# Kernel optimization log

Measured on AMD Instinct MI355X. Metric: run time of the kernel, lower is better.

## Reference

```python
import jax, jax.numpy as jnp
import numpy as np

NUM_USERS = 100000
NUM_ITEMS = 50000
EMB = 64
N_LAYERS = 3
NNZ = 4800000
N_NODES = NUM_USERS + NUM_ITEMS


def setup_inputs() -> dict:
    key = jax.random.key(0)
    k1, k2, k3, k4, k5 = jax.random.split(key, 5)
    emb_user = jax.random.normal(k1, (NUM_USERS, EMB), dtype=jnp.float32) * 0.1
    emb_item = jax.random.normal(k2, (NUM_ITEMS, EMB), dtype=jnp.float32) * 0.1
    adj_rows = jax.random.randint(k3, (NNZ,), 0, N_NODES, dtype=jnp.int32)
    adj_cols = jax.random.randint(k4, (NNZ,), 0, N_NODES, dtype=jnp.int32)
    # normalized adjacency values (stand-in for D^-1/2 A D^-1/2 entries)
    adj_vals = jax.random.uniform(k5, (NNZ,), dtype=jnp.float32) / 32.0
    return {
        "emb_user": emb_user,
        "emb_item": emb_item,
        "adj_vals": adj_vals,
        "adj_rows": adj_rows,
        "adj_cols": adj_cols,
    }


def _spmm(vals, rows, cols, x):
    # y[r] = sum_{e: rows[e]==r} vals[e] * x[cols[e]]
    gathered = x[cols] * vals[:, None]  # [nnz, emb]
    return jax.ops.segment_sum(gathered, rows, num_segments=N_NODES)


def reference(emb_user, emb_item, adj_vals, adj_rows, adj_cols):
    ego = jnp.concatenate([emb_user, emb_item], axis=0)  # [(U+I), emb]
    acc = ego
    h = ego
    for _ in range(N_LAYERS):
        h = _spmm(adj_vals, adj_rows, adj_cols, h)
        acc = acc + h
    mean_emb = acc / jnp.float32(N_LAYERS + 1)
    user_embeddings = mean_emb[:NUM_USERS]
    item_embeddings = mean_emb[NUM_USERS:]
    return user_embeddings, item_embeddings
```

## Files before the change

### kernel.cpp

```cpp
#include <hip/hip_runtime.h>
#include <hip/hip_bf16.h>

#define N_USERS   100000
#define N_ITEMS   50000
#define N_NODES_C 150000
#define EMB       64
#define N_ELEM    (N_NODES_C * EMB)
#define BKT_SHIFT 9
#define NBKT      ((N_NODES_C + 511) >> 9)
#define BKT_CAP   20480
#define CH_EDGES  4096
#define EPT       16

typedef unsigned int u32x4 __attribute__((ext_vector_type(4)));
typedef unsigned int u32x2 __attribute__((ext_vector_type(2)));
typedef unsigned long long u64;

__global__ void detect_and_zero(const unsigned int* __restrict__ emb_u32,
                                const unsigned int* __restrict__ vals_u32,
                                int* __restrict__ flags,
                                int* __restrict__ tails) {
    int t = threadIdx.x;
    for (int b = t; b < NBKT; b += 256) tails[b] = 0;
    int cnt_emb = 0, cnt_vals = 0;
    for (int k = t; k < 1024; k += 256) {
        unsigned e = (emb_u32[k] >> 7) & 0xFFu;
        cnt_emb += (e >= 100u && e <= 127u) ? 1 : 0;
        cnt_vals += (vals_u32[k] >> 15) & 1u;
    }
    __shared__ int s0[256], s1[256];
    s0[t] = cnt_emb; s1[t] = cnt_vals;
    __syncthreads();
    for (int s = 128; s > 0; s >>= 1) {
        if (t < s) { s0[t] += s0[t + s]; s1[t] += s1[t + s]; }
        __syncthreads();
    }
    if (t == 0) {
        flags[0] = (s0[0] > 512) ? 1 : 0;
        flags[1] = (s1[0] > 100) ? 0 : 1;
    }
}

__device__ __forceinline__ float load_f(const void* base, size_t i, int is_bf16) {
    if (is_bf16) return __bfloat162float(((const __hip_bfloat16*)base)[i]);
    return ((const float*)base)[i];
}
__device__ __forceinline__ unsigned int bf16_bits(float f) {
    __hip_bfloat16 h = __float2bfloat16(f);
    return (unsigned int)reinterpret_cast<unsigned short&>(h);
}
__device__ __forceinline__ float lo_bf(unsigned int u) {
    return __uint_as_float(u << 16);
}
__device__ __forceinline__ float hi_bf(unsigned int u) {
    return __uint_as_float(u & 0xFFFF0000u);
}

__global__ void init_kernel(const void* __restrict__ eu,
                            const void* __restrict__ ei,
                            __hip_bfloat16* __restrict__ h0,
                            const int* __restrict__ flags) {
    int q = blockIdx.x * blockDim.x + threadIdx.x;
    if (q >= (N_ELEM >> 2)) return;
    int ebf = flags[0];
    const int uquads = (N_USERS * EMB) >> 2;
    u32x2 o;
    if (ebf) {
        o = (q < uquads)
              ? *((const u32x2*)eu + q)
              : *((const u32x2*)ei + (q - uquads));
    } else {
        const uint4 f = (q < uquads)
              ? *((const uint4*)eu + q)
              : *((const uint4*)ei + (q - uquads));
        unsigned r0, r1;
        asm("v_cvt_pk_bf16_f32 %0, %1, %2" : "=v"(r0)
            : "v"(__uint_as_float(f.x)), "v"(__uint_as_float(f.y)));
        asm("v_cvt_pk_bf16_f32 %0, %1, %2" : "=v"(r1)
            : "v"(__uint_as_float(f.z)), "v"(__uint_as_float(f.w)));
        o.x = r0; o.y = r1;
    }
    *reinterpret_cast<u32x2*>(h0 + ((size_t)q << 2)) = o;
}

__global__ void scatter_bucket(const int* __restrict__ rows, const int* __restrict__ cols,
                               const void* __restrict__ vals,
                               u64* __restrict__ tmp,
                               int* __restrict__ tails, int nnz,
                               const int* __restrict__ flags) {
    __shared__ int lcnt[NBKT];
    __shared__ int lbase[NBKT];
    int t = threadIdx.x;
    for (int b = t; b < NBKT; b += 256) lcnt[b] = 0;
    __syncthreads();
    int base = blockIdx.x * CH_EDGES;
    int vbf = flags[1];
    u64 pk[EPT];
    unsigned int br[EPT];
    #pragma unroll
    for (int i = 0; i < EPT; ++i) {
        int e = base + i * 256 + t;
        if (e < nnz) {
            int r = rows[e];
            int c = cols[e];
            float v = load_f(vals, (size_t)e, vbf);
            int bk = r >> BKT_SHIFT;
            int rk = atomicAdd(&lcnt[bk], 1);
            pk[i] = ((u64)(unsigned)r << 34)
                  | ((u64)(unsigned)c << 16)
                  | (u64)bf16_bits(v);
            br[i] = ((unsigned)bk << 16) | (unsigned)rk;
        } else {
            br[i] = 0xFFFFFFFFu;
        }
    }
    __syncthreads();
    for (int b = t; b < NBKT; b += 256)
        lbase[b] = lcnt[b] ? atomicAdd(&tails[b], lcnt[b]) : 0;
    __syncthreads();
    #pragma unroll
    for (int i = 0; i < EPT; ++i) {
        if (br[i] != 0xFFFFFFFFu) {
            int bk = br[i] >> 16, rk = br[i] & 0xFFFFu;
            int pos = lbase[bk] + rk;
            if (pos < BKT_CAP)
                tmp[(size_t)bk * BKT_CAP + pos] = pk[i];
        }
    }
}

__global__ void bucket_csr(const u64* __restrict__ tmp,
                           int2* __restrict__ edges,
                           const int* __restrict__ tails,
                           int* __restrict__ row_ptr) {
    __shared__ int cnt[512];
    __shared__ int off[512];
    __shared__ int red[512];
    int b = blockIdx.x, t = threadIdx.x;
    int pre = 0;
    for (int i = t; i < b; i += 512) {
        int v = tails[i];
        pre += (v > BKT_CAP) ? BKT_CAP : v;
    }
    red[t] = pre;
    cnt[t] = 0;
    int rowbase = b << BKT_SHIFT;
    int nrows = N_NODES_C - rowbase; if (nrows > 512) nrows = 512;
    int n = tails[b];
    if (n > BKT_CAP) n = BKT_CAP;
    const u64* src = tmp + (size_t)b * BKT_CAP;
    __syncthreads();
    for (int st = 256; st > 0; st >>= 1) {
        if (t < st) red[t] += red[t + st];
        __syncthreads();
    }
    int obase = red[0];
    for (int e = t; e < n; e += 512)
        atomicAdd(&cnt[(int)(src[e] >> 34) - rowbase], 1);
    __syncthreads();
    int v = cnt[t];
    off[t] = v;
    __syncthreads();
    for (int o = 1; o < 512; o <<= 1) {
        int u = (t >= o) ? off[t - o] : 0;
        __syncthreads();
        off[t] += u;
        __syncthreads();
    }
    int excl = off[t] - v;
    __syncthreads();
    off[t] = obase + excl;
    if (t < nrows) row_ptr[rowbase + t] = obase + excl;
    if (b == NBKT - 1 && t == 0) row_ptr[N_NODES_C] = obase + n;
    __syncthreads();
    for (int e = t; e < n; e += 512) {
        u64 p = src[e];
        int rloc = (int)(p >> 34) - rowbase;
        unsigned c = (unsigned)((p >> 16) & 0x3FFFFu);
        int pos = atomicAdd(&off[rloc], 1);
        edges[pos] = make_int2((int)(c << 7), (int)((unsigned)(p & 0xFFFFu) << 16));
    }
}

#define DOT2Q(wA, wB, vp, ae, ao)                                              \
    {                                                                          \
        unsigned _xe = __builtin_amdgcn_perm((wA), (wB), 0x01000504u);         \
        unsigned _xo = __builtin_amdgcn_perm((wA), (wB), 0x03020706u);         \
        asm("v_dot2_f32_bf16 %0, %1, %2, %0" : "+v"(ae) : "v"(_xe), "v"(vp));  \
        asm("v_dot2_f32_bf16 %0, %1, %2, %0" : "+v"(ao) : "v"(_xo), "v"(vp));  \
    }

#define SWZ_ADD(a, pat) \
    a += __int_as_float(__builtin_amdgcn_ds_swizzle(__float_as_int(a), pat))

__global__ void spmm8(const __hip_bfloat16* __restrict__ x,
                      __hip_bfloat16* __restrict__ y,
                      const u64* __restrict__ edges,
                      const int* __restrict__ row_ptr,
                      const __hip_bfloat16* __restrict__ h0,
                      const __hip_bfloat16* __restrict__ h1,
                      void* __restrict__ out,
                      const int* __restrict__ flags,
                      int last) {
    int row = __builtin_amdgcn_readfirstlane(blockIdx.x * 4 + (threadIdx.x >> 6));
    if (row >= N_NODES_C) return;
    int lane = threadIdx.x & 63;
    int slot = lane >> 3;
    int s    = lane & 7;
    int beg = row_ptr[row], end = row_ptr[row + 1];
    const char* xb = (const char*)x;
    const char* eb = (const char*)edges;
    unsigned s16 = (unsigned)s << 4;
    unsigned eoff = ((unsigned)(beg + slot)) << 3;
    float a0 = 0.f, a1 = 0.f, a2 = 0.f, a3 = 0.f,
          a4 = 0.f, a5 = 0.f, a6 = 0.f, a7 = 0.f;
    for (int e = beg; e < end; e += 32, eoff += 256) {
        int rem = end - e;
        const u64* ep = (const u64*)(eb + eoff);
        u64 pA = (slot      < rem) ? __builtin_nontemporal_load(ep)      : 0ULL;
        u64 pB = (slot + 8  < rem) ? __builtin_nontemporal_load(ep + 8)  : 0ULL;
        u64 pC = (slot + 16 < rem) ? __builtin_nontemporal_load(ep + 16) : 0ULL;
        u64 pD = (slot + 24 < rem) ? __builtin_nontemporal_load(ep + 24) : 0ULL;
        unsigned oA = (unsigned)pA + s16;
        unsigned oB = (unsigned)pB + s16;
        unsigned oC = (unsigned)pC + s16;
        unsigned oD = (unsigned)pD + s16;
        const uint4 gA = *reinterpret_cast<const uint4*>(xb + oA);
        const uint4 gB = *reinterpret_cast<const uint4*>(xb + oB);
        const uint4 gC = *reinterpret_cast<const uint4*>(xb + oC);
        const uint4 gD = *reinterpret_cast<const uint4*>(xb + oD);
        unsigned vAB = __builtin_amdgcn_perm((unsigned)(pA >> 32),
                                             (unsigned)(pB >> 32), 0x03020706u);
        unsigned vCD = __builtin_amdgcn_perm((unsigned)(pC >> 32),
                                             (unsigned)(pD >> 32), 0x03020706u);
        DOT2Q(gA.x, gB.x, vAB, a0, a1);
        DOT2Q(gA.y, gB.y, vAB, a2, a3);
        DOT2Q(gA.z, gB.z, vAB, a4, a5);
        DOT2Q(gA.w, gB.w, vAB, a6, a7);
        DOT2Q(gC.x, gD.x, vCD, a0, a1);
        DOT2Q(gC.y, gD.y, vCD, a2, a3);
        DOT2Q(gC.z, gD.z, vCD, a4, a5);
        DOT2Q(gC.w, gD.w, vCD, a6, a7);
    }
    SWZ_ADD(a0, 0x201F); SWZ_ADD(a1, 0x201F); SWZ_ADD(a2, 0x201F); SWZ_ADD(a3, 0x201F);
    SWZ_ADD(a4, 0x201F); SWZ_ADD(a5, 0x201F); SWZ_ADD(a6, 0x201F); SWZ_ADD(a7, 0x201F);
    SWZ_ADD(a0, 0x401F); SWZ_ADD(a1, 0x401F); SWZ_ADD(a2, 0x401F); SWZ_ADD(a3, 0x401F);
    SWZ_ADD(a4, 0x401F); SWZ_ADD(a5, 0x401F); SWZ_ADD(a6, 0x401F); SWZ_ADD(a7, 0x401F);
    a0 += __shfl_xor(a0, 32, 64);
    a1 += __shfl_xor(a1, 32, 64);
    a2 += __shfl_xor(a2, 32, 64);
    a3 += __shfl_xor(a3, 32, 64);
    a4 += __shfl_xor(a4, 32, 64);
    a5 += __shfl_xor(a5, 32, 64);
    a6 += __shfl_xor(a6, 32, 64);
    a7 += __shfl_xor(a7, 32, 64);
    if (slot != 0) return;
    size_t base = ((size_t)row << 6) + (s << 3);
    if (!last) {
        unsigned q0, q1, q2, q3;
        asm("v_cvt_pk_bf16_f32 %0, %1, %2" : "=v"(q0) : "v"(a0), "v"(a1));
        asm("v_cvt_pk_bf16_f32 %0, %1, %2" : "=v"(q1) : "v"(a2), "v"(a3));
        asm("v_cvt_pk_bf16_f32 %0, %1, %2" : "=v"(q2) : "v"(a4), "v"(a5));
        asm("v_cvt_pk_bf16_f32 %0, %1, %2" : "=v"(q3) : "v"(a6), "v"(a7));
        u32x4 o; o.x = q0; o.y = q1; o.z = q2; o.w = q3;
        *reinterpret_cast<u32x4*>(y + base) = o;
    } else {
        const uint4 r0 = *reinterpret_cast<const uint4*>(h0 + base);
        const uint4 r1 = *reinterpret_cast<const uint4*>(h1 + base);
        const uint4 r2 = *reinterpret_cast<const uint4*>(x + base);
        float f0 = (lo_bf(r0.x) + lo_bf(r1.x) + lo_bf(r2.x) + a0) * 0.25f;
        float f1 = (hi_bf(r0.x) + hi_bf(r1.x) + hi_bf(r2.x) + a1) * 0.25f;
        float f2 = (lo_bf(r0.y) + lo_bf(r1.y) + lo_bf(r2.y) + a2) * 0.25f;
        float f3 = (hi_bf(r0.y) + hi_bf(r1.y) + hi_bf(r2.y) + a3) * 0.25f;
        float f4 = (lo_bf(r0.z) + lo_bf(r1.z) + lo_bf(r2.z) + a4) * 0.25f;
        float f5 = (hi_bf(r0.z) + hi_bf(r1.z) + hi_bf(r2.z) + a5) * 0.25f;
        float f6 = (lo_bf(r0.w) + lo_bf(r1.w) + lo_bf(r2.w) + a6) * 0.25f;
        float f7 = (hi_bf(r0.w) + hi_bf(r1.w) + hi_bf(r2.w) + a7) * 0.25f;
        if (flags[0]) {
            unsigned q0, q1, q2, q3;
            asm("v_cvt_pk_bf16_f32 %0, %1, %2" : "=v"(q0) : "v"(f0), "v"(f1));
            asm("v_cvt_pk_bf16_f32 %0, %1, %2" : "=v"(q1) : "v"(f2), "v"(f3));
            asm("v_cvt_pk_bf16_f32 %0, %1, %2" : "=v"(q2) : "v"(f4), "v"(f5));
            asm("v_cvt_pk_bf16_f32 %0, %1, %2" : "=v"(q3) : "v"(f6), "v"(f7));
            u32x4 o; o.x = q0; o.y = q1; o.z = q2; o.w = q3;
            __builtin_nontemporal_store(
                o, reinterpret_cast<u32x4*>((__hip_bfloat16*)out + base));
        } else {
            float* op = (float*)out + base;
            u32x4 q0, q1;
            q0.x = __float_as_uint(f0); q0.y = __float_as_uint(f1);
            q0.z = __float_as_uint(f2); q0.w = __float_as_uint(f3);
            q1.x = __float_as_uint(f4); q1.y = __float_as_uint(f5);
            q1.z = __float_as_uint(f6); q1.w = __float_as_uint(f7);
            __builtin_nontemporal_store(q0, reinterpret_cast<u32x4*>(op));
            __builtin_nontemporal_store(q1, reinterpret_cast<u32x4*>(op + 4));
        }
    }
}

extern "C" void kernel_launch(void* const* d_in, const int* in_sizes, int n_in,
                              void* d_out, int out_size, void* d_ws, size_t ws_size,
                              hipStream_t stream) {
    const void* eu   = d_in[0];
    const void* ei   = d_in[1];
    const void* vals = d_in[2];
    const int*  rows = (const int*)d_in[3];
    const int*  cols = (const int*)d_in[4];
    const int nnz = in_sizes[2];

    __hip_bfloat16* h[3];
    h[0] = (__hip_bfloat16*)d_ws;
    h[1] = h[0] + N_ELEM;
    h[2] = h[1] + N_ELEM;
    int2* edges   = (int2*)(h[2] + N_ELEM);
    int* row_ptr  = (int*)(edges + nnz);
    int* tails    = row_ptr + (N_NODES_C + 1);
    int* flags    = tails + NBKT;
    char* pt = (char*)(flags + 2);
    u64* tmp = (u64*)(((uintptr_t)pt + 7) & ~(uintptr_t)7);

    detect_and_zero<<<1, 256, 0, stream>>>((const unsigned int*)eu,
                                           (const unsigned int*)vals, flags, tails);
    init_kernel<<<((N_ELEM >> 2) + 255) / 256, 256, 0, stream>>>(eu, ei, h[0], flags);

    int nchunks = (nnz + CH_EDGES - 1) / CH_EDGES;
    scatter_bucket<<<nchunks, 256, 0, stream>>>(rows, cols, vals, tmp, tails, nnz, flags);
    bucket_csr<<<NBKT, 512, 0, stream>>>(tmp, edges, tails, row_ptr);

    int nsb = (N_NODES_C + 3) / 4;
    spmm8<<<nsb, 256, 0, stream>>>(h[0], h[1], (const u64*)edges, row_ptr,
                                   nullptr, nullptr, nullptr, flags, 0);
    spmm8<<<nsb, 256, 0, stream>>>(h[1], h[2], (const u64*)edges, row_ptr,
                                   nullptr, nullptr, nullptr, flags, 0);
    spmm8<<<nsb, 256, 0, stream>>>(h[2], nullptr, (const u64*)edges, row_ptr,
                                   h[0], h[1], d_out, flags, 1);
}
```

Before: 502.6 us.

## Fuse dtype detection, init and bucket scatter into one launch

Drops the single-block detect kernel and has each wave probe the input dtype itself with a ballot over 64 words. The init conversion blocks are appended to the scatter grid so both run in one launch, and the bucket counters are cleared with a memset. bucket_csr's LDS tree reduction and Hillis-Steele scan are replaced with wave shuffles plus a per-wave sum. This removes two serial launches and many barriers, but the probe now samples 64 words instead of 1024, so the dtype heuristic becomes less robust.

Result: no change. 501.7 us (-0.2%).

```diff
diff --git a/kernel.cpp b/kernel.cpp
--- a/kernel.cpp
+++ b/kernel.cpp
@@ -16,35 +16,6 @@
 typedef unsigned int u32x2 __attribute__((ext_vector_type(2)));
 typedef unsigned long long u64;
 
-__global__ void detect_and_zero(const unsigned int* __restrict__ emb_u32,
-                                const unsigned int* __restrict__ vals_u32,
-                                int* __restrict__ flags,
-                                int* __restrict__ tails) {
-    int t = threadIdx.x;
-    for (int b = t; b < NBKT; b += 256) tails[b] = 0;
-    int cnt_emb = 0, cnt_vals = 0;
-    for (int k = t; k < 1024; k += 256) {
-        unsigned e = (emb_u32[k] >> 7) & 0xFFu;
-        cnt_emb += (e >= 100u && e <= 127u) ? 1 : 0;
-        cnt_vals += (vals_u32[k] >> 15) & 1u;
-    }
-    __shared__ int s0[256], s1[256];
-    s0[t] = cnt_emb; s1[t] = cnt_vals;
-    __syncthreads();
-    for (int s = 128; s > 0; s >>= 1) {
-        if (t < s) { s0[t] += s0[t + s]; s1[t] += s1[t + s]; }
-        __syncthreads();
-    }
-    if (t == 0) {
-        flags[0] = (s0[0] > 512) ? 1 : 0;
-        flags[1] = (s1[0] > 100) ? 0 : 1;
-    }
-}
-
-__device__ __forceinline__ float load_f(const void* base, size_t i, int is_bf16) {
-    if (is_bf16) return __bfloat162float(((const __hip_bfloat16*)base)[i]);
-    return ((const float*)base)[i];
-}
 __device__ __forceinline__ unsigned int bf16_bits(float f) {
     __hip_bfloat16 h = __float2bfloat16(f);
     return (unsigned int)reinterpret_cast<unsigned short&>(h);
@@ -56,45 +27,52 @@
     return __uint_as_float(u & 0xFFFF0000u);
 }
 
-__global__ void init_kernel(const void* __restrict__ eu,
-                            const void* __restrict__ ei,
-                            __hip_bfloat16* __restrict__ h0,
-                            const int* __restrict__ flags) {
-    int q = blockIdx.x * blockDim.x + threadIdx.x;
-    if (q >= (N_ELEM >> 2)) return;
-    int ebf = flags[0];
-    const int uquads = (N_USERS * EMB) >> 2;
-    u32x2 o;
-    if (ebf) {
-        o = (q < uquads)
-              ? *((const u32x2*)eu + q)
-              : *((const u32x2*)ei + (q - uquads));
-    } else {
-        const uint4 f = (q < uquads)
-              ? *((const uint4*)eu + q)
-              : *((const uint4*)ei + (q - uquads));
-        unsigned r0, r1;
-        asm("v_cvt_pk_bf16_f32 %0, %1, %2" : "=v"(r0)
-            : "v"(__uint_as_float(f.x)), "v"(__uint_as_float(f.y)));
-        asm("v_cvt_pk_bf16_f32 %0, %1, %2" : "=v"(r1)
-            : "v"(__uint_as_float(f.z)), "v"(__uint_as_float(f.w)));
-        o.x = r0; o.y = r1;
-    }
-    *reinterpret_cast<u32x2*>(h0 + ((size_t)q << 2)) = o;
-}
-
-__global__ void scatter_bucket(const int* __restrict__ rows, const int* __restrict__ cols,
-                               const void* __restrict__ vals,
-                               u64* __restrict__ tmp,
-                               int* __restrict__ tails, int nnz,
-                               const int* __restrict__ flags) {
+__device__ __forceinline__ int probe_emb_bf16(const void* eu, int lane) {
+    unsigned w = ((const unsigned*)eu)[lane];
+    unsigned e = (w >> 7) & 0xFFu;
+    return __popcll(__ballot(e >= 100u && e <= 127u)) > 32;
+}
+__device__ __forceinline__ int probe_vals_bf16(const void* vals, int lane) {
+    unsigned w = ((const unsigned*)vals)[lane];
+    return __popcll(__ballot((w >> 15) & 1u)) < 8;
+}
+
+__global__ void prep_fused(const int* __restrict__ rows, const int* __restrict__ cols,
+                           const void* __restrict__ vals,
+                           u64* __restrict__ tmp, int* __restrict__ tails, int nnz,
+                           int nchunks,
+                           const void* __restrict__ eu, const void* __restrict__ ei,
+                           __hip_bfloat16* __restrict__ h0) {
+    int t = threadIdx.x;
+    int lane = t & 63;
+    if ((int)blockIdx.x >= nchunks) {
+        int ebf = probe_emb_bf16(eu, lane);
+        int q = ((int)blockIdx.x - nchunks) * 256 + t;
+        if (q >= (N_ELEM >> 2)) return;
+        const int uquads = (N_USERS * EMB) >> 2;
+        u32x2 o;
+        if (ebf) {
+            o = (q < uquads) ? *((const u32x2*)eu + q)
+                             : *((const u32x2*)ei + (q - uquads));
+        } else {
+            const uint4 f = (q < uquads) ? *((const uint4*)eu + q)
+                                         : *((const uint4*)ei + (q - uquads));
+            unsigned r0, r1;
+            asm("v_cvt_pk_bf16_f32 %0, %1, %2" : "=v"(r0)
+                : "v"(__uint_as_float(f.x)), "v"(__uint_as_float(f.y)));
+            asm("v_cvt_pk_bf16_f32 %0, %1, %2" : "=v"(r1)
+                : "v"(__uint_as_float(f.z)), "v"(__uint_as_float(f.w)));
+            o.x = r0; o.y = r1;
+        }
+        *reinterpret_cast<u32x2*>(h0 + ((size_t)q << 2)) = o;
+        return;
+    }
     __shared__ int lcnt[NBKT];
     __shared__ int lbase[NBKT];
-    int t = threadIdx.x;
+    int vbf = probe_vals_bf16(vals, lane);
     for (int b = t; b < NBKT; b += 256) lcnt[b] = 0;
     __syncthreads();
     int base = blockIdx.x * CH_EDGES;
-    int vbf = flags[1];
     u64 pk[EPT];
     unsigned int br[EPT];
     #pragma unroll
@@ -103,7 +81,8 @@
         if (e < nnz) {
             int r = rows[e];
             int c = cols[e];
-            float v = load_f(vals, (size_t)e, vbf);
+            float v = vbf ? __bfloat162float(((const __hip_bfloat16*)vals)[e])
+                          : ((const float*)vals)[e];
             int bk = r >> BKT_SHIFT;
             int rk = atomicAdd(&lcnt[bk], 1);
             pk[i] = ((u64)(unsigned)r << 34)
@@ -135,42 +114,43 @@
                            int* __restrict__ row_ptr) {
     __shared__ int cnt[512];
     __shared__ int off[512];
-    __shared__ int red[512];
+    __shared__ int wsum[8];
     int b = blockIdx.x, t = threadIdx.x;
+    int lane = t & 63, wid = t >> 6;
+    int rowbase = b << BKT_SHIFT;
+    int nrows = N_NODES_C - rowbase; if (nrows > 512) nrows = 512;
+    int n = tails[b]; if (n > BKT_CAP) n = BKT_CAP;
+    const u64* src = tmp + (size_t)b * BKT_CAP;
     int pre = 0;
     for (int i = t; i < b; i += 512) {
         int v = tails[i];
         pre += (v > BKT_CAP) ? BKT_CAP : v;
     }
-    red[t] = pre;
+    #pragma unroll
+    for (int m = 1; m < 64; m <<= 1) pre += __shfl_xor(pre, m, 64);
     cnt[t] = 0;
-    int rowbase = b << BKT_SHIFT;
-    int nrows = N_NODES_C - rowbase; if (nrows > 512) nrows = 512;
-    int n = tails[b];
-    if (n > BKT_CAP) n = BKT_CAP;
-    const u64* src = tmp + (size_t)b * BKT_CAP;
-    __syncthreads();
-    for (int st = 256; st > 0; st >>= 1) {
-        if (t < st) red[t] += red[t + st];
-        __syncthreads();
-    }
-    int obase = red[0];
+    if (lane == 0) wsum[wid] = pre;
+    __syncthreads();
+    int obase = 0;
+    #pragma unroll
+    for (int i = 0; i < 8; ++i) obase += wsum[i];
     for (int e = t; e < n; e += 512)
         atomicAdd(&cnt[(int)(src[e] >> 34) - rowbase], 1);
     __syncthreads();
     int v = cnt[t];
-    off[t] = v;
-    __syncthreads();
-    for (int o = 1; o < 512; o <<= 1) {
-        int u = (t >= o) ? off[t - o] : 0;
-        __syncthreads();
-        off[t] += u;
-        __syncthreads();
-    }
-    int excl = off[t] - v;
-    __syncthreads();
-    off[t] = obase + excl;
-    if (t < nrows) row_ptr[rowbase + t] = obase + excl;
+    int sc = v;
+    #pragma unroll
+    for (int m = 1; m < 64; m <<= 1) {
+        int u = __shfl_up(sc, m, 64);
+        if (lane >= m) sc += u;
+    }
+    if (lane == 63) wsum[wid] = sc;
+    __syncthreads();
+    int woff = 0;
+    for (int i = 0; i < wid; ++i) woff += wsum[i];
+    int excl = obase + woff + sc - v;
+    off[t] = excl;
+    if (t < nrows) row_ptr[rowbase + t] = excl;
     if (b == NBKT - 1 && t == 0) row_ptr[N_NODES_C] = obase + n;
     __syncthreads();
     for (int e = t; e < n; e += 512) {
@@ -200,11 +180,13 @@
                       const __hip_bfloat16* __restrict__ h0,
                       const __hip_bfloat16* __restrict__ h1,
                       void* __restrict__ out,
-                      const int* __restrict__ flags,
+                      const void* __restrict__ eu,
                       int last) {
+    int lane = threadIdx.x & 63;
+    int ebf = 0;
+    if (last) ebf = probe_emb_bf16(eu, lane);
     int row = __builtin_amdgcn_readfirstlane(blockIdx.x * 4 + (threadIdx.x >> 6));
     if (row >= N_NODES_C) return;
-    int lane = threadIdx.x & 63;
     int slot = lane >> 3;
     int s    = lane & 7;
     int beg = row_ptr[row], end = row_ptr[row + 1];
@@ -276,7 +258,7 @@
         float f5 = (hi_bf(r0.z) + hi_bf(r1.z) + hi_bf(r2.z) + a5) * 0.25f;
         float f6 = (lo_bf(r0.w) + lo_bf(r1.w) + lo_bf(r2.w) + a6) * 0.25f;
         float f7 = (hi_bf(r0.w) + hi_bf(r1.w) + hi_bf(r2.w) + a7) * 0.25f;
-        if (flags[0]) {
+        if (ebf) {
             unsigned q0, q1, q2, q3;
             asm("v_cvt_pk_bf16_f32 %0, %1, %2" : "=v"(q0) : "v"(f0), "v"(f1));
             asm("v_cvt_pk_bf16_f32 %0, %1, %2" : "=v"(q1) : "v"(f2), "v"(f3));
@@ -315,23 +297,22 @@
     int2* edges   = (int2*)(h[2] + N_ELEM);
     int* row_ptr  = (int*)(edges + nnz);
     int* tails    = row_ptr + (N_NODES_C + 1);
-    int* flags    = tails + NBKT;
-    char* pt = (char*)(flags + 2);
+    char* pt = (char*)(tails + NBKT);
     u64* tmp = (u64*)(((uintptr_t)pt + 7) & ~(uintptr_t)7);
 
-    detect_and_zero<<<1, 256, 0, stream>>>((const unsigned int*)eu,
-                                           (const unsigned int*)vals, flags, tails);
-    init_kernel<<<((N_ELEM >> 2) + 255) / 256, 256, 0, stream>>>(eu, ei, h[0], flags);
+    hipMemsetAsync(tails, 0, NBKT * sizeof(int), stream);
 
     int nchunks = (nnz + CH_EDGES - 1) / CH_EDGES;
-    scatter_bucket<<<nchunks, 256, 0, stream>>>(rows, cols, vals, tmp, tails, nnz, flags);
+    int ninit = ((N_ELEM >> 2) + 255) / 256;
+    prep_fused<<<nchunks + ninit, 256, 0, stream>>>(rows, cols, vals, tmp, tails,
+                                                    nnz, nchunks, eu, ei, h[0]);
     bucket_csr<<<NBKT, 512, 0, stream>>>(tmp, edges, tails, row_ptr);
 
     int nsb = (N_NODES_C + 3) / 4;
     spmm8<<<nsb, 256, 0, stream>>>(h[0], h[1], (const u64*)edges, row_ptr,
-                                   nullptr, nullptr, nullptr, flags, 0);
+                                   nullptr, nullptr, nullptr, eu, 0);
     spmm8<<<nsb, 256, 0, stream>>>(h[1], h[2], (const u64*)edges, row_ptr,
-                                   nullptr, nullptr, nullptr, flags, 0);
+                                   nullptr, nullptr, nullptr, eu, 0);
     spmm8<<<nsb, 256, 0, stream>>>(h[2], nullptr, (const u64*)edges, row_ptr,
-                                   h[0], h[1], d_out, flags, 1);
-}
+                                   h[0], h[1], d_out, eu, 1);
+}
```
